# Performance work log

Hardware: AMD Instinct MI355X
Metric: run time of the kernel (lower is better)

The kernel has to match this reference:

```python
import jax, jax.numpy as jnp
import numpy as np

VOCAB = 50257
DIM = 1024
B, S = 4, 4096


def setup_inputs() -> dict:
    key = jax.random.key(0)
    k1, k2, k3 = jax.random.split(key, 3)
    input_ids = jax.random.randint(k1, (B, S), 0, VOCAB)
    weight = jax.random.normal(k2, (VOCAB, DIM), dtype=jnp.float32)
    # R initialized as a random matrix stand-in for the learned Stiefel rotation
    R = jax.random.normal(k3, (DIM, DIM), dtype=jnp.float32) / np.sqrt(DIM)
    return {"input_ids": input_ids, "weight": weight, "R": R}


def reference(input_ids, weight, R):
    # Faithful to the module: rotate the FULL embedding table, then gather.
    w_eff = weight @ R              # [V, D] @ [D, D] -> [V, D]
    return jnp.take(w_eff, input_ids, axis=0)  # [B, S, D]
```

## Files before the change

kernel.cpp:

```cpp
#include <hip/hip_runtime.h>
#include <hip/hip_bf16.h>


typedef __attribute__((ext_vector_type(4))) float f32x4;
typedef __attribute__((ext_vector_type(8))) short s16x8;
typedef __attribute__((ext_vector_type(2))) int i32x2;

#define DIM 1024
#define NTK 32

__device__ __forceinline__ short f2bf(float f) {
  unsigned u = __float_as_uint(f);
  unsigned r = (u + 0x7FFFu + ((u >> 16) & 1u)) >> 16;
  return (short)r;
}

__device__ __forceinline__ void gload_lds16(const void* g, void* l) {
  __builtin_amdgcn_global_load_lds((const __attribute__((address_space(1))) void*)g,
                                   (__attribute__((address_space(3))) void*)l, 16, 0, 0);
}

__global__ __launch_bounds__(256) void prep_kernel(const float* __restrict__ R,
                                                   short* __restrict__ RT,
                                                   const float* __restrict__ W,
                                                   const int* __restrict__ ids,
                                                   short* __restrict__ G) {
  const int b = blockIdx.x;
  const int t = threadIdx.x;
  if (b < 1024) {
    __shared__ float tile[32][33];
    const int bx = b & 31, by = b >> 5;
    const int tx = t & 31, ty = t >> 5;
#pragma unroll
    for (int i = 0; i < 4; ++i)
      tile[ty + i * 8][tx] = R[(size_t)(by * 32 + ty + i * 8) * DIM + bx * 32 + tx];
    __syncthreads();
#pragma unroll
    for (int i = 0; i < 4; ++i)
      RT[(size_t)(bx * 32 + ty + i * 8) * DIM + by * 32 + tx] = f2bf(tile[tx][ty + i * 8]);
  } else {
    const int tid = (b - 1024) * 256 + t;
#pragma unroll
    for (int i = 0; i < 8; ++i) {
      const int g = tid + i * (2048 * 256);
      const int row = g >> 8;
      const int c4 = (g & 255) << 2;
      const f32x4 v = *(const f32x4*)(W + (size_t)ids[row] * DIM + c4);
      i32x2 p;
      p[0] = (int)(unsigned short)f2bf(v[0]) | ((int)f2bf(v[1]) << 16);
      p[1] = (int)(unsigned short)f2bf(v[2]) | ((int)f2bf(v[3]) << 16);
      *(i32x2*)(G + (size_t)g * 4) = p;
    }
  }
}

__global__ __launch_bounds__(512, 4) void rot_embed_gemm(const short* __restrict__ G,
                                                         const short* __restrict__ RT,
                                                         float* __restrict__ out) {
  extern __shared__ char smem[];

  const int t = threadIdx.x;
  const int b = blockIdx.x;
  const int swz = (b & 7) * 64 + (b >> 3);
  const int m0 = (swz >> 2) * 128;
  const int n0 = (swz & 3) * 256;

  const int lane = t & 63;
  const int w = t >> 6;
  const int wm = w >> 2, wn = w & 3;
  const int fr = lane & 15, fq = lane >> 4;

  char* const ldsA = smem;
  char* const ldsB = smem + 24576;

  const int arow = t >> 2;
  const int achk = ((t & 3) ^ (arow & 3)) * 8;
  const short* gA = G + (size_t)(m0 + arow) * DIM + achk;
  const short* gB0 = RT + (size_t)(n0 + arow) * DIM + achk;
  const short* gB1 = RT + (size_t)(n0 + 128 + arow) * DIM + achk;
  const int dOff = w * 1024;

#define STA(buf, kt) gload_lds16(gA + (kt) * 32, ldsA + (buf) * 8192 + dOff)
#define STB(buf, kt)                                                   \
  {                                                                    \
    gload_lds16(gB0 + (kt) * 32, ldsB + (buf) * 16384 + dOff);         \
    gload_lds16(gB1 + (kt) * 32, ldsB + (buf) * 16384 + 8192 + dOff);  \
  }

  f32x4 acc[4][4];
#pragma unroll
  for (int i = 0; i < 4; ++i)
#pragma unroll
    for (int j = 0; j < 4; ++j) acc[i][j] = (f32x4)0.0f;

  const int sl = (fq ^ (fr & 3)) << 4;

  STA(0, 0);
  STB(0, 0);
  STA(1, 1);

  int bA = 0, bB = 0;
  for (int kt = 0; kt < NTK; ++kt) {
    if (kt == NTK - 1)
      asm volatile("s_waitcnt vmcnt(0)" ::: "memory");
    else
      asm volatile("s_waitcnt vmcnt(1)" ::: "memory");
    asm volatile("s_waitcnt lgkmcnt(0)" ::: "memory");
    __builtin_amdgcn_s_barrier();

    if (kt + 1 < NTK) STB(bB ^ 1, kt + 1);
    if (kt + 2 < NTK) { const int nb = (bA + 2 >= 3) ? bA - 1 : bA + 2; STA(nb, kt + 2); }

    const char* A = ldsA + bA * 8192;
    const char* B = ldsB + bB * 16384;
    s16x8 af[4], bfv[4];
#pragma unroll
    for (int i = 0; i < 4; ++i) {
      af[i] = *(const s16x8*)(A + (wm * 64 + i * 16 + fr) * 64 + sl);
      bfv[i] = *(const s16x8*)(B + (wn * 64 + i * 16 + fr) * 64 + sl);
    }
#pragma unroll
    for (int mi = 0; mi < 4; ++mi)
#pragma unroll
      for (int nj = 0; nj < 4; ++nj)
        acc[mi][nj] = __builtin_amdgcn_mfma_f32_16x16x32_bf16(af[mi], bfv[nj], acc[mi][nj], 0, 0, 0);

    bA = (bA + 1 == 3) ? 0 : bA + 1;
    bB ^= 1;
  }

#pragma unroll
  for (int mi = 0; mi < 4; ++mi)
#pragma unroll
    for (int nj = 0; nj < 4; ++nj) {
      float* op = out + (size_t)(m0 + wm * 64 + mi * 16 + fq * 4) * DIM +
                  (n0 + wn * 64 + nj * 16 + fr);
#pragma unroll
      for (int r = 0; r < 4; ++r)
        __builtin_nontemporal_store(acc[mi][nj][r], op + (size_t)r * DIM);
    }
#undef STA
#undef STB
}

extern "C" void kernel_launch(void* const* d_in, const int* in_sizes, int n_in,
                              void* d_out, int out_size, void* d_ws, size_t ws_size,
                              hipStream_t stream) {
  const int* ids = (const int*)d_in[0];
  const float* W = (const float*)d_in[1];
  const float* R = (const float*)d_in[2];
  float* out = (float*)d_out;
  short* RT = (short*)d_ws;
  short* G = (short*)d_ws + (size_t)DIM * DIM;

  prep_kernel<<<dim3(3072), dim3(256), 0, stream>>>(R, RT, W, ids, G);
  rot_embed_gemm<<<dim3(512), dim3(512), 57344, stream>>>(G, RT, out);
}
```

Measured before the change: 67.54 us.

## Shrink GEMM tile to 128x128 with 256 threads and triple-buffer both operands

Reworks the GEMM block tile from 128x256 with 8 waves to 128x128 with 4 waves, launching 1024 blocks instead of 512. Both A and B tiles are now triple-buffered with a unified load macro and a new three-way XOR swizzle for LDS. It also raises wave priority around the MFMA block. The aim is better occupancy and load balance across CUs, at the cost of less B reuse per block and more global traffic for R.

```diff
diff --git a/kernel.cpp b/kernel.cpp
--- a/kernel.cpp
+++ b/kernel.cpp
@@ -54,37 +54,38 @@
   }
 }
 
-__global__ __launch_bounds__(512, 4) void rot_embed_gemm(const short* __restrict__ G,
+__global__ __launch_bounds__(256, 3) void rot_embed_gemm(const short* __restrict__ G,
                                                          const short* __restrict__ RT,
                                                          float* __restrict__ out) {
   extern __shared__ char smem[];
 
   const int t = threadIdx.x;
   const int b = blockIdx.x;
-  const int swz = (b & 7) * 64 + (b >> 3);
-  const int m0 = (swz >> 2) * 128;
-  const int n0 = (swz & 3) * 256;
+  const int swz = (b & 7) * 128 + (b >> 3);
+  const int m0 = (swz >> 3) * 128;
+  const int n0 = (swz & 7) * 128;
 
   const int lane = t & 63;
   const int w = t >> 6;
-  const int wm = w >> 2, wn = w & 3;
+  const int wm = w >> 1, wn = w & 1;
   const int fr = lane & 15, fq = lane >> 4;
 
   char* const ldsA = smem;
   char* const ldsB = smem + 24576;
 
-  const int arow = t >> 2;
-  const int achk = ((t & 3) ^ (arow & 3)) * 8;
-  const short* gA = G + (size_t)(m0 + arow) * DIM + achk;
-  const short* gB0 = RT + (size_t)(n0 + arow) * DIM + achk;
-  const short* gB1 = RT + (size_t)(n0 + 128 + arow) * DIM + achk;
+  const int scol = ((t & 3) ^ ((t >> 2) & 3) ^ ((t >> 4) & 3)) * 8;
+  const short* gA = G + (size_t)(m0 + (t >> 2)) * DIM + scol;
+  const short* gB = RT + (size_t)(n0 + (t >> 2)) * DIM + scol;
   const int dOff = w * 1024;
 
-#define STA(buf, kt) gload_lds16(gA + (kt) * 32, ldsA + (buf) * 8192 + dOff)
-#define STB(buf, kt)                                                   \
-  {                                                                    \
-    gload_lds16(gB0 + (kt) * 32, ldsB + (buf) * 16384 + dOff);         \
-    gload_lds16(gB1 + (kt) * 32, ldsB + (buf) * 16384 + 8192 + dOff);  \
+#define STG(buf, kt)                                                       \
+  {                                                                        \
+    gload_lds16(gA + (kt) * 32, ldsA + (buf) * 8192 + dOff);               \
+    gload_lds16(gA + (size_t)64 * DIM + (kt) * 32,                         \
+                ldsA + (buf) * 8192 + 4096 + dOff);                        \
+    gload_lds16(gB + (kt) * 32, ldsB + (buf) * 8192 + dOff);               \
+    gload_lds16(gB + (size_t)64 * DIM + (kt) * 32,                         \
+                ldsB + (buf) * 8192 + 4096 + dOff);                        \
   }
 
   f32x4 acc[4][4];
@@ -93,40 +94,36 @@
 #pragma unroll
     for (int j = 0; j < 4; ++j) acc[i][j] = (f32x4)0.0f;
 
-  const int sl = (fq ^ (fr & 3)) << 4;
+  const int sl = ((fq ^ (fr & 3) ^ ((fr >> 2) & 3)) & 3) << 4;
 
-  STA(0, 0);
-  STB(0, 0);
-  STA(1, 1);
+  STG(0, 0);
+  STG(1, 1);
 
-  int bA = 0, bB = 0;
   for (int kt = 0; kt < NTK; ++kt) {
     if (kt == NTK - 1)
       asm volatile("s_waitcnt vmcnt(0)" ::: "memory");
     else
-      asm volatile("s_waitcnt vmcnt(1)" ::: "memory");
+      asm volatile("s_waitcnt vmcnt(4)" ::: "memory");
     asm volatile("s_waitcnt lgkmcnt(0)" ::: "memory");
     __builtin_amdgcn_s_barrier();
 
-    if (kt + 1 < NTK) STB(bB ^ 1, kt + 1);
-    if (kt + 2 < NTK) { const int nb = (bA + 2 >= 3) ? bA - 1 : bA + 2; STA(nb, kt + 2); }
+    if (kt + 2 < NTK) STG((kt + 2) % 3, kt + 2);
 
-    const char* A = ldsA + bA * 8192;
-    const char* B = ldsB + bB * 16384;
+    const char* A = ldsA + (kt % 3) * 8192;
+    const char* B = ldsB + (kt % 3) * 8192;
     s16x8 af[4], bfv[4];
 #pragma unroll
     for (int i = 0; i < 4; ++i) {
       af[i] = *(const s16x8*)(A + (wm * 64 + i * 16 + fr) * 64 + sl);
       bfv[i] = *(const s16x8*)(B + (wn * 64 + i * 16 + fr) * 64 + sl);
     }
+    __builtin_amdgcn_s_setprio(1);
 #pragma unroll
     for (int mi = 0; mi < 4; ++mi)
 #pragma unroll
       for (int nj = 0; nj < 4; ++nj)
         acc[mi][nj] = __builtin_amdgcn_mfma_f32_16x16x32_bf16(af[mi], bfv[nj], acc[mi][nj], 0, 0, 0);
-
-    bA = (bA + 1 == 3) ? 0 : bA + 1;
-    bB ^= 1;
+    __builtin_amdgcn_s_setprio(0);
   }
 
 #pragma unroll
@@ -139,8 +136,7 @@
       for (int r = 0; r < 4; ++r)
         __builtin_nontemporal_store(acc[mi][nj][r], op + (size_t)r * DIM);
     }
-#undef STA
-#undef STB
+#undef STG
 }
 
 extern "C" void kernel_launch(void* const* d_in, const int* in_sizes, int n_in,
@@ -154,5 +150,5 @@
   short* G = (short*)d_ws + (size_t)DIM * DIM;
 
   prep_kernel<<<dim3(3072), dim3(256), 0, stream>>>(R, RT, W, ids, G);
-  rot_embed_gemm<<<dim3(512), dim3(512), 57344, stream>>>(G, RT, out);
+  rot_embed_gemm<<<dim3(1024), dim3(256), 49152, stream>>>(G, RT, out);
 }
```

Measured after the change: 66.67 us. About the same (-1.3%).
